# Performance work log

Measured on AMD Instinct MI355X. Metric: run time of the kernel, lower is better.

Reference implementation:

```python
import jax, jax.numpy as jnp
import numpy as np

H, NH, L, S, B, V = 512, 8, 6, 2048, 2, 32000
DH = H // NH
EPS = 1e-5


def posenc(h, s):
    pos = jnp.arange(s, dtype=jnp.float32)[:, None]
    div = jnp.power(10000.0, jnp.arange(0, h, 2, dtype=jnp.float32) / h)
    pe = jnp.zeros((s, h), dtype=jnp.float32)
    pe = pe.at[:, 0::2].set(jnp.sin(pos / div))
    pe = pe.at[:, 1::2].set(jnp.cos(pos / div))
    return pe


def layernorm(x, g, b):
    mu = jnp.mean(x, axis=-1, keepdims=True)
    var = jnp.mean(jnp.square(x - mu), axis=-1, keepdims=True)
    return (x - mu) * jax.lax.rsqrt(var + EPS) * g + b


def setup_inputs() -> dict:
    key = jax.random.key(0)
    ks = jax.random.split(key, 16)
    sc = 0.02
    return {
        "src": jax.random.randint(ks[0], (B, S), 0, V),
        "mask": jnp.ones((B, 1, 1, S), dtype=jnp.int32),
        "emb": jax.random.normal(ks[1], (V, H), jnp.float32) * sc,
        "Wq": jax.random.normal(ks[2], (L, H, H), jnp.float32) * sc,
        "bq": jnp.zeros((L, H), jnp.float32),
        "Wk": jax.random.normal(ks[3], (L, H, H), jnp.float32) * sc,
        "bk": jnp.zeros((L, H), jnp.float32),
        "Wv": jax.random.normal(ks[4], (L, H, H), jnp.float32) * sc,
        "bv": jnp.zeros((L, H), jnp.float32),
        "Wo": jax.random.normal(ks[5], (L, H, H), jnp.float32) * sc,
        "bo": jnp.zeros((L, H), jnp.float32),
        "gamma": jnp.ones((L, H), jnp.float32),
        "beta": jnp.zeros((L, H), jnp.float32),
        "W1": jax.random.normal(ks[6], (L, H, 4 * H), jnp.float32) * sc,
        "b1": jnp.zeros((L, 4 * H), jnp.float32),
        "W2": jax.random.normal(ks[7], (L, 4 * H, H), jnp.float32) * sc,
        "b2": jnp.zeros((L, H), jnp.float32),
    }


def reference(src, mask, emb, Wq, bq, Wk, bk, Wv, bv, Wo, bo, gamma, beta, W1, b1, W2, b2):
    x = emb[src] + posenc(H, S)[None, :, :]  # [B,S,H]
    for i in range(L):
        q = (x @ Wq[i] + bq[i]).reshape(B, S, NH, DH).transpose(0, 2, 1, 3)
        k = (x @ Wk[i] + bk[i]).reshape(B, S, NH, DH).transpose(0, 2, 1, 3)
        v = (x @ Wv[i] + bv[i]).reshape(B, S, NH, DH).transpose(0, 2, 1, 3)
        scores = jnp.einsum("bhqd,bhkd->bhqk", q, k) / jnp.sqrt(jnp.float32(DH))
        scores = jnp.where(mask == 0, jnp.float32(-1e20), scores)
        attn = jax.nn.softmax(scores, axis=-1)
        av = jnp.einsum("bhqk,bhkd->bhqd", attn, v)
        attn_out = av.transpose(0, 2, 1, 3).reshape(B, S, H) @ Wo[i] + bo[i]
        # NOTE: same LayerNorm params applied to both sublayers (as in source)
        res = x + layernorm(attn_out, gamma[i], beta[i])
        ffn = jax.nn.relu(res @ W1[i] + b1[i]) @ W2[i] + b2[i]
        x = res + layernorm(ffn, gamma[i], beta[i])
    return x
```

## Files before the change

kernel.cpp:

```cpp
#include <hip/hip_runtime.h>
#include <math.h>

#define HDIM 512
#define NHEAD 8
#define NLAYER 6
#define SEQ 2048
#define BATCH 2
#define DHEAD 64
#define TOKENS (BATCH*SEQ)
#define FFND (4*HDIM)
#define QSTR 1536

typedef unsigned short u16;
typedef unsigned long long u64;
typedef __attribute__((ext_vector_type(8))) short short8;
typedef __attribute__((ext_vector_type(4))) float f32x4;

__device__ __forceinline__ u16 f2b(float f) {
  unsigned u = __float_as_uint(f);
  u += 0x7FFFu + ((u >> 16) & 1u);
  return (u16)(u >> 16);
}

__device__ __forceinline__ unsigned cvtpk_bf16(float lo, float hi) {
  unsigned r;
  asm("v_cvt_pk_bf16_f32 %0, %1, %2" : "=v"(r) : "v"(lo), "v"(hi));
  return r;
}

__device__ __forceinline__ void gload_lds16(const u16* g, u16* l) {
  __builtin_amdgcn_global_load_lds((const __attribute__((address_space(1))) void*)g,
                                   (__attribute__((address_space(3))) void*)l, 16, 0, 0);
}

__global__ void embed_pe(const int* __restrict__ src, const float* __restrict__ emb,
                         float* __restrict__ X, u16* __restrict__ Xb) {
  int tok = blockIdx.x;
  int lane = threadIdx.x;
  int s = tok & (SEQ - 1);
  int c0 = lane * 8;
  const float* e = emb + (long)src[tok] * HDIM + c0;
  float v[8];
#pragma unroll
  for (int j = 0; j < 8; j++) {
    int c = c0 + j;
    float arg = (float)s * exp2f(-(float)(c & ~1) * 0.02595256917f);
    v[j] = e[j] + ((c & 1) ? cosf(arg) : sinf(arg));
  }
  float* xp = X + (long)tok * HDIM + c0;
#pragma unroll
  for (int j = 0; j < 8; j++) xp[j] = v[j];
  u16 hb[8];
#pragma unroll
  for (int j = 0; j < 8; j++) hb[j] = f2b(v[j]);
  uint4 pk;
  pk.x = hb[0] | ((unsigned)hb[1] << 16);
  pk.y = hb[2] | ((unsigned)hb[3] << 16);
  pk.z = hb[4] | ((unsigned)hb[5] << 16);
  pk.w = hb[6] | ((unsigned)hb[7] << 16);
  *(uint4*)(Xb + (long)tok * HDIM + c0) = pk;
}

__global__ void maskprep(const int* __restrict__ mask, u64* __restrict__ mb) {
  int t = threadIdx.x;
  int b = t >> 5, tile = t & 31;
  const int* m = mask + b * SEQ + tile * 64;
  u64 w = 0;
#pragma unroll
  for (int j = 0; j < 64; j++) w |= (u64)(m[j] != 0) << j;
  mb[t] = w;
}

__global__ __launch_bounds__(256) void prep_weights(
    const float* __restrict__ Wq, const float* __restrict__ Wk, const float* __restrict__ Wv,
    const float* __restrict__ Wo, const float* __restrict__ W1, const float* __restrict__ W2,
    const float* __restrict__ bq, const float* __restrict__ bk, const float* __restrict__ bv,
    u16* __restrict__ Wqkvt, u16* __restrict__ Wot, u16* __restrict__ W1t, u16* __restrict__ W2t,
    float* __restrict__ bqkv) {
  int t = blockIdx.x;
  int tid = threadIdx.x;
  if (t == 768) {
    for (int i = tid; i < 1536; i += 256)
      bqkv[i] = (i < 512) ? bq[i] : (i < 1024) ? bk[i - 512] : bv[i - 1024];
    return;
  }
  const float* src; u16* dst; int K, N, kt, nt; long drow0 = 0;
  if (t < 192)      { int m = t / 64, r = t % 64; src = (m==0)?Wq:(m==1)?Wk:Wv; dst = Wqkvt; drow0 = (long)m*512; K=512;  N=512;  kt=r/8;  nt=r%8; }
  else if (t < 256) { int r = t - 192; src = Wo; dst = Wot; K=512;  N=512;  kt=r/8;  nt=r%8; }
  else if (t < 512) { int r = t - 256; src = W1; dst = W1t; K=512;  N=2048; kt=r/32; nt=r%32; }
  else              { int r = t - 512; src = W2; dst = W2t; K=2048; N=512;  kt=r/8;  nt=r%8; }
  __shared__ __align__(16) u16 Lt[64 * 72];
  int kl = tid >> 2;
#pragma unroll
  for (int rr = 0; rr < 4; rr++) {
    int cl = (tid & 3) * 4 + rr * 16;
    float4 v = *(const float4*)(src + (long)(kt * 64 + kl) * N + nt * 64 + cl);
    Lt[(cl + 0) * 72 + kl] = f2b(v.x);
    Lt[(cl + 1) * 72 + kl] = f2b(v.y);
    Lt[(cl + 2) * 72 + kl] = f2b(v.z);
    Lt[(cl + 3) * 72 + kl] = f2b(v.w);
  }
  __syncthreads();
  int nl = tid >> 2;
  int kc = (tid & 3) * 16;
  u16* dp = dst + (drow0 + nt * 64 + nl) * (long)K + kt * 64 + kc;
  *(uint4*)dp       = *(const uint4*)&Lt[nl * 72 + kc];
  *(uint4*)(dp + 8) = *(const uint4*)&Lt[nl * 72 + kc + 8];
}

__global__ __launch_bounds__(256) void vtranspose(const u16* __restrict__ QKV,
                                                  u16* __restrict__ Vtb) {
  __shared__ __align__(16) u16 Lt[64 * 72];
  int tid = threadIdx.x;
  int bh = blockIdx.y, b = bh >> 3, h = bh & 7;
  int s0 = blockIdx.x * 64;
  const u16* vsrc = QKV + (long)(b * SEQ + s0) * QSTR + 1024 + h * DHEAD;
  int key = tid >> 2, dc = (tid & 3) * 16;
  const u16* vp = vsrc + (long)key * QSTR + dc;
  uint4 v0 = *(const uint4*)vp;
  uint4 v1 = *(const uint4*)(vp + 8);
  unsigned vr[8] = { v0.x, v0.y, v0.z, v0.w, v1.x, v1.y, v1.z, v1.w };
#pragma unroll
  for (int j = 0; j < 8; j++) {
    Lt[(dc + 2 * j) * 72 + key]     = (u16)vr[j];
    Lt[(dc + 2 * j + 1) * 72 + key] = (u16)(vr[j] >> 16);
  }
  __syncthreads();
  int d = tid >> 2, kc = (tid & 3) * 16;
  u16* dst = Vtb + ((long)bh * DHEAD + d) * SEQ + s0 + kc;
  *(uint4*)dst       = *(const uint4*)&Lt[d * 72 + kc];
  *(uint4*)(dst + 8) = *(const uint4*)&Lt[d * 72 + kc + 8];
}

template <int BN, int KSPLIT, bool RELU, bool WF32, bool WB16>
__global__ __launch_bounds__(256) void gemm_tn(const u16* __restrict__ A,
                                               const u16* __restrict__ Bt,
                                               const float* __restrict__ bias,
                                               float* __restrict__ Cf,
                                               u16* __restrict__ Cb,
                                               int M, int N, int K) {
  constexpr int NF = BN / 32;
  __shared__ __align__(16) u16 As[2][128 * 32];
  __shared__ __align__(16) u16 Bs[2][BN * 32];
  int tid = threadIdx.x;
  int wave = tid >> 6, lane = tid & 63;
  int ln = lane & 15, hi = lane >> 4;
  int wm = wave >> 1, wn = wave & 1;
  int m0 = blockIdx.y * 128, n0 = blockIdx.x * BN;
  int z = (KSPLIT > 1) ? blockIdx.z : 0;
  int Ks = K / KSPLIT;
  const u16* Ab = A + z * Ks;
  const u16* Bb = Bt + z * Ks;

  f32x4 acc[4][NF] = {};

  int srow = lane >> 2;
  int skc  = (lane & 3) * 8;

  auto issue = [&](int kt, int buf) {
    int k0 = kt * 32;
#pragma unroll
    for (int j = 0; j < 2; j++) {
      int row = (wave * 2 + j) * 16 + srow;
      gload_lds16(Ab + (long)(m0 + row) * K + k0 + skc, &As[buf][row * 32 + skc]);
    }
#pragma unroll
    for (int j = 0; j < BN / 64; j++) {
      int row = (wave * (BN / 64) + j) * 16 + srow;
      gload_lds16(Bb + (long)(n0 + row) * K + k0 + skc, &Bs[buf][row * 32 + skc]);
    }
  };

  int NT = Ks / 32;
  issue(0, 0);
  __syncthreads();
  for (int kt = 0; kt < NT; kt++) {
    int buf = kt & 1;
    if (kt + 1 < NT) issue(kt + 1, buf ^ 1);
    short8 af[4], bf[NF];
#pragma unroll
    for (int mt = 0; mt < 4; mt++)
      af[mt] = *(const short8*)&As[buf][(wm * 64 + mt * 16 + ln) * 32 + 8 * hi];
#pragma unroll
    for (int nt = 0; nt < NF; nt++)
      bf[nt] = *(const short8*)&Bs[buf][(wn * (BN / 2) + nt * 16 + ln) * 32 + 8 * hi];
#pragma unroll
    for (int mt = 0; mt < 4; mt++)
#pragma unroll
      for (int nt = 0; nt < NF; nt++)
        acc[mt][nt] = __builtin_amdgcn_mfma_f32_16x16x32_bf16(af[mt], bf[nt], acc[mt][nt], 0, 0, 0);
    __syncthreads();
  }

  float* Cz = WF32 ? (Cf + (long)z * M * N) : nullptr;
#pragma unroll
  for (int mt = 0; mt < 4; mt++)
#pragma unroll
    for (int nt = 0; nt < NF; nt++)
#pragma unroll
      for (int r = 0; r < 4; r++) {
        int row = m0 + wm * 64 + mt * 16 + hi * 4 + r;
        int col = n0 + wn * (BN / 2) + nt * 16 + ln;
        float v = acc[mt][nt][r];
        if (KSPLIT == 1 || z == 0) v += bias[col];
        if (RELU) v = fmaxf(v, 0.0f);
        if (WF32) Cz[(long)row * N + col] = v;
        if (WB16) Cb[(long)row * N + col] = f2b(v);
      }
}

__global__ __launch_bounds__(256) void attention(const u16* __restrict__ QKV,
                                                 const u16* __restrict__ Vtb,
                                                 const u64* __restrict__ maskb,
                                                 float* __restrict__ Opart,
                                                 float* __restrict__ Lpart) {
  __shared__ __align__(16) u16 Ks[2][64 * 64];
  __shared__ __align__(16) u16 Vs[2][64 * 64];
  __shared__ u64 Msk[SEQ / 64];
  int tid = threadIdx.x, w = tid >> 6, lane = tid & 63;
  int ln = lane & 15, hi = lane >> 4;
  int h0 = hi & 1, h1 = hi >> 1, ln7 = ln & 7;
  int lin = blockIdx.x;
  int lid = (lin & 7) * 128 + (lin >> 3);
  int bh = lid >> 6, qt = (lid >> 1) & 31, kz = lid & 1;
  int b = bh >> 3, h = bh & 7;
  int q0 = qt * 64 + w * 16;
  const u16* qbase = QKV + (long)b * SEQ * QSTR + h * DHEAD;
  const u16* kbase = qbase + 512;
  const u16* vtbase = Vtb + (long)bh * DHEAD * SEQ;

  short8 qf[2];
#pragma unroll
  for (int ks = 0; ks < 2; ks++)
    qf[ks] = *(const short8*)(qbase + (long)(q0 + ln) * QSTR + ks * 32 + 8 * hi);

  u64 mw0 = 0;
  if (tid < SEQ / 64) mw0 = maskb[b * (SEQ / 64) + tid];

  int sr0 = tid >> 3, sc = tid & 7;
  const u16 *kp0, *kp1, *vp0, *vp1;
  {
    int r1 = sr0 + 32;
    int key0 = (sr0 & 7) | ((sr0 & 0x18) << 1) | ((sr0 & 0x20) >> 2);
    int key1 = (r1 & 7) | ((r1 & 0x18) << 1) | ((r1 & 0x20) >> 2);
    kp0 = kbase + (long)key0 * QSTR + (sc ^ (sr0 & 7)) * 8;
    kp1 = kbase + (long)key1 * QSTR + (sc ^ (r1 & 7)) * 8;
    vp0 = vtbase + (long)sr0 * SEQ + (sc ^ (sr0 & 7)) * 8;
    vp1 = vtbase + (long)r1 * SEQ + (sc ^ (r1 & 7)) * 8;
  }
  int d0 = sr0 * 64 + sc * 8, d1 = d0 + 2048;

  auto issue = [&](int t, int buf) {
    long ko = (long)t * (64 * QSTR);
    int vo = t * 64;
    gload_lds16(kp0 + ko, &Ks[buf][d0]);
    gload_lds16(kp1 + ko, &Ks[buf][d1]);
    gload_lds16(vp0 + vo, &Vs[buf][d0]);
    gload_lds16(vp1 + vo, &Vs[buf][d1]);
  };

  f32x4 o[4] = {};
  float lsum = 0.0f;
  const int t0 = kz * 16;
  const int NTL = 16;

  issue(t0, 0);
  issue(t0 + 1, 1);
  if (tid < SEQ / 64) Msk[tid] = mw0;
  asm volatile("s_waitcnt vmcnt(4)" ::: "memory");
  __builtin_amdgcn_sched_barrier(0);
  __builtin_amdgcn_s_barrier();
  __builtin_amdgcn_sched_barrier(0);

  for (int ti = 0; ti < NTL; ti++) {
    int buf = ti & 1;
    u64 mw = Msk[t0 + ti];

    f32x4 s[4] = {};
#pragma unroll
    for (int ks = 0; ks < 2; ks++)
#pragma unroll
      for (int kb = 0; kb < 4; kb++) {
        short8 kf = *(const short8*)&Ks[buf][(kb * 16 + ln) * 64 + (((ks << 2) + hi) ^ ln7) * 8];
        s[kb] = __builtin_amdgcn_mfma_f32_16x16x32_bf16(kf, qf[ks], s[kb], 0, 0, 0);
      }

    unsigned D[4][2];
    if (mw == 0xFFFFFFFFFFFFFFFFull) {
#pragma unroll
      for (int kb = 0; kb < 4; kb++) {
        float p[4];
#pragma unroll
        for (int r = 0; r < 4; r++) {
          float pv = __expf(s[kb][r] * 0.125f);
          lsum += pv;
          p[r] = pv;
        }
        D[kb][0] = cvtpk_bf16(p[0], p[1]);
        D[kb][1] = cvtpk_bf16(p[2], p[3]);
      }
    } else {
      unsigned shb = h1 * 16 + h0 * 4;
      u64 mws = mw >> shb;
      unsigned nib[4] = { (unsigned)mws & 0xFu, (unsigned)(mws >> 32) & 0xFu,
                          (unsigned)(mws >> 8) & 0xFu, (unsigned)(mws >> 40) & 0xFu };
#pragma unroll
      for (int kb = 0; kb < 4; kb++) {
        float p[4];
#pragma unroll
        for (int r = 0; r < 4; r++) {
          float pv = __expf(s[kb][r] * 0.125f);
          pv = ((nib[kb] >> r) & 1u) ? pv : 0.0f;
          lsum += pv;
          p[r] = pv;
        }
        D[kb][0] = cvtpk_bf16(p[0], p[1]);
        D[kb][1] = cvtpk_bf16(p[2], p[3]);
      }
    }

    short8 pb[2];
#pragma unroll
    for (int ks = 0; ks < 2; ks++) {
      unsigned own0 = h0 ? D[2 + ks][0] : D[ks][0];
      unsigned own1 = h0 ? D[2 + ks][1] : D[ks][1];
      unsigned snd0 = h0 ? D[ks][0] : D[2 + ks][0];
      unsigned snd1 = h0 ? D[ks][1] : D[2 + ks][1];
      unsigned rc0 = (unsigned)__shfl_xor((int)snd0, 16);
      unsigned rc1 = (unsigned)__shfl_xor((int)snd1, 16);
      union { unsigned u[4]; short8 v; } pu;
      pu.u[0] = h0 ? rc0 : own0;
      pu.u[1] = h0 ? rc1 : own1;
      pu.u[2] = h0 ? own0 : rc0;
      pu.u[3] = h0 ? own1 : rc1;
      pb[ks] = pu.v;
    }

#pragma unroll
    for (int ks = 0; ks < 2; ks++)
#pragma unroll
      for (int mb = 0; mb < 4; mb++) {
        short8 vf = *(const short8*)&Vs[buf][(mb * 16 + ln) * 64 + (((ks << 2) + hi) ^ ln7) * 8];
        o[mb] = __builtin_amdgcn_mfma_f32_16x16x32_bf16(vf, pb[ks], o[mb], 0, 0, 0);
      }

    asm volatile("s_waitcnt lgkmcnt(0)" ::: "memory");
    __builtin_amdgcn_sched_barrier(0);
    __builtin_amdgcn_s_barrier();
    __builtin_amdgcn_sched_barrier(0);
    if (ti + 2 < NTL) {
      issue(t0 + ti + 2, buf);
      asm volatile("s_waitcnt vmcnt(4)" ::: "memory");
    } else {
      asm volatile("s_waitcnt vmcnt(0)" ::: "memory");
    }
    __builtin_amdgcn_sched_barrier(0);
    __builtin_amdgcn_s_barrier();
    __builtin_amdgcn_sched_barrier(0);
  }

  lsum += __shfl_xor(lsum, 16);
  lsum += __shfl_xor(lsum, 32);

  float* OpB = Opart + (long)lid * 4096 + w * 1024;
#pragma unroll
  for (int mb = 0; mb < 4; mb++)
    *(f32x4*)&OpB[ln * 64 + mb * 16 + hi * 4] = o[mb];
  if (hi == 0) Lpart[(long)lid * 64 + w * 16 + ln] = lsum;
}

__global__ __launch_bounds__(256) void attn_merge(const float* __restrict__ Op,
                                                  const float* __restrict__ Lp,
                                                  u16* __restrict__ Og) {
  int lin = blockIdx.x;
  int mlid = (lin & 7) * 64 + (lin >> 3);
  int bh = mlid >> 5, qt = mlid & 31;
  int b = bh >> 3, h = bh & 7;
  int tid = threadIdx.x;
  __shared__ float Ls[64];
  if (tid < 64) Ls[tid] = 1.0f / (Lp[(long)mlid * 128 + tid] + Lp[(long)mlid * 128 + 64 + tid]);
  __syncthreads();
  const float* P0 = Op + (long)mlid * 8192;
  const float* P1 = P0 + 4096;
  u16* obase = Og + (long)b * SEQ * HDIM + (long)qt * 64 * HDIM + h * DHEAD;
#pragma unroll
  for (int j = 0; j < 4; j++) {
    int flat = j * 1024 + tid * 4;
    int row = flat >> 6, c = flat & 63;
    float4 a = *(const float4*)&P0[flat];
    float4 bb = *(const float4*)&P1[flat];
    float rl = Ls[row];
    uint2 val;
    val.x = cvtpk_bf16((a.x + bb.x) * rl, (a.y + bb.y) * rl);
    val.y = cvtpk_bf16((a.z + bb.z) * rl, (a.w + bb.w) * rl);
    *(uint2*)(obase + (long)row * HDIM + c) = val;
  }
}

__global__ __launch_bounds__(256) void ln_residual(const float* __restrict__ Xin,
                                                   const float* __restrict__ T0,
                                                   const float* __restrict__ T1,
                                                   const float* __restrict__ gamma,
                                                   const float* __restrict__ beta,
                                                   float* __restrict__ Xout,
                                                   u16* __restrict__ Xb) {
  int tid = threadIdx.x, w = tid >> 6, lane = tid & 63;
  int row = blockIdx.x * 4 + w;
  const float* t0 = T0 + (long)row * HDIM;
  const float* t1 = T1 + (long)row * HDIM;
  int c0 = lane * 8;
  float v[8];
  {
    float4 a0 = *(const float4*)(t0 + c0);
    float4 b0 = *(const float4*)(t0 + c0 + 4);
    float4 a1 = *(const float4*)(t1 + c0);
    float4 b1 = *(const float4*)(t1 + c0 + 4);
    v[0] = a0.x + a1.x; v[1] = a0.y + a1.y; v[2] = a0.z + a1.z; v[3] = a0.w + a1.w;
    v[4] = b0.x + b1.x; v[5] = b0.y + b1.y; v[6] = b0.z + b1.z; v[7] = b0.w + b1.w;
  }
  float sum = 0.0f;
#pragma unroll
  for (int j = 0; j < 8; j++) sum += v[j];
#pragma unroll
  for (int off = 32; off; off >>= 1) sum += __shfl_xor(sum, off);
  float mu = sum * (1.0f / HDIM);
  float sq = 0.0f;
#pragma unroll
  for (int j = 0; j < 8; j++) { float d = v[j] - mu; sq += d * d; }
#pragma unroll
  for (int off = 32; off; off >>= 1) sq += __shfl_xor(sq, off);
  float rs = rsqrtf(sq * (1.0f / HDIM) + 1e-5f);
  const float* xin = Xin + (long)row * HDIM + c0;
  float* xout = Xout + (long)row * HDIM + c0;
  u16 hb[8];
#pragma unroll
  for (int j = 0; j < 8; j++) {
    int c = c0 + j;
    float y = xin[j] + (v[j] - mu) * rs * gamma[c] + beta[c];
    xout[j] = y;
    hb[j] = f2b(y);
  }
  uint4 pk;
  pk.x = hb[0] | ((unsigned)hb[1] << 16);
  pk.y = hb[2] | ((unsigned)hb[3] << 16);
  pk.z = hb[4] | ((unsigned)hb[5] << 16);
  pk.w = hb[6] | ((unsigned)hb[7] << 16);
  *(uint4*)(Xb + (long)row * HDIM + c0) = pk;
}

extern "C" void kernel_launch(void* const* d_in, const int* in_sizes, int n_in,
                              void* d_out, int out_size, void* d_ws, size_t ws_size,
                              hipStream_t stream) {
  const int*   src   = (const int*)d_in[0];
  const int*   mask  = (const int*)d_in[1];
  const float* emb   = (const float*)d_in[2];
  const float* Wq    = (const float*)d_in[3];
  const float* bq    = (const float*)d_in[4];
  const float* Wk    = (const float*)d_in[5];
  const float* bk    = (const float*)d_in[6];
  const float* Wv    = (const float*)d_in[7];
  const float* bv    = (const float*)d_in[8];
  const float* Wo    = (const float*)d_in[9];
  const float* bo    = (const float*)d_in[10];
  const float* gamma = (const float*)d_in[11];
  const float* beta  = (const float*)d_in[12];
  const float* W1    = (const float*)d_in[13];
  const float* b1    = (const float*)d_in[14];
  const float* W2    = (const float*)d_in[15];
  const float* b2    = (const float*)d_in[16];

  char* ws = (char*)d_ws;
  float* X     = (float*)(ws);
  u16*   Xb    = (u16*)(ws + (8ll << 20));
  u16*   QKVb  = (u16*)(ws + (12ll << 20));
  u16*   Mb    = (u16*)(ws + (12ll << 20));
  u16*   AVb   = (u16*)(ws + (24ll << 20));
  float* T     = (float*)(ws + (28ll << 20));
  u16*   Wqkvt = (u16*)(ws + (44ll << 20));
  u16*   Wot   = (u16*)(ws + (45ll << 20) + (512ll << 10));
  u16*   W1t   = (u16*)(ws + (46ll << 20));
  u16*   W2t   = (u16*)(ws + (48ll << 20));
  float* bqkv  = (float*)(ws + (50ll << 20));
  float* Lpart = (float*)(ws + (50ll << 20) + (512ll << 10));
  u16*   Vtb   = (u16*)(ws + (51ll << 20));
  u64*   maskbits = (u64*)(ws + (55ll << 20));
  float* Opart = T;
  float* T1    = T + (long)TOKENS * HDIM;

  embed_pe<<<dim3(TOKENS), dim3(64), 0, stream>>>(src, emb, X, Xb);
  maskprep<<<dim3(1), dim3(64), 0, stream>>>(mask, maskbits);

  for (int i = 0; i < NLAYER; i++) {
    long wo = (long)i * HDIM * HDIM;
    prep_weights<<<dim3(769), 256, 0, stream>>>(
        Wq + wo, Wk + wo, Wv + wo, Wo + wo,
        W1 + (long)i * HDIM * FFND, W2 + (long)i * FFND * HDIM,
        bq + i * HDIM, bk + i * HDIM, bv + i * HDIM,
        Wqkvt, Wot, W1t, W2t, bqkv);

    gemm_tn<128, 1, false, false, true><<<dim3(QSTR / 128, TOKENS / 128), 256, 0, stream>>>(
        Xb, Wqkvt, bqkv, nullptr, QKVb, TOKENS, QSTR, HDIM);

    vtranspose<<<dim3(SEQ / 64, BATCH * NHEAD), 256, 0, stream>>>(QKVb, Vtb);

    attention<<<dim3(1024), 256, 0, stream>>>(QKVb, Vtb, maskbits, Opart, Lpart);

    attn_merge<<<dim3(512), 256, 0, stream>>>(Opart, Lpart, AVb);

    gemm_tn<64, 2, false, true, false><<<dim3(HDIM / 64, TOKENS / 128, 2), 256, 0, stream>>>(
        AVb, Wot, bo + i * HDIM, T, nullptr, TOKENS, HDIM, HDIM);

    ln_residual<<<dim3(TOKENS / 4), 256, 0, stream>>>(X, T, T1, gamma + i * HDIM,
                                                      beta + i * HDIM, X, Xb);

    gemm_tn<128, 1, true, false, true><<<dim3(FFND / 128, TOKENS / 128), 256, 0, stream>>>(
        Xb, W1t, b1 + (long)i * FFND, nullptr, Mb, TOKENS, FFND, HDIM);

    gemm_tn<64, 2, false, true, false><<<dim3(HDIM / 64, TOKENS / 128, 2), 256, 0, stream>>>(
        Mb, W2t, b2 + i * HDIM, T, nullptr, TOKENS, HDIM, FFND);

    ln_residual<<<dim3(TOKENS / 4), 256, 0, stream>>>(X, T, T1, gamma + i * HDIM,
                                                      beta + i * HDIM, X, Xb);
  }

  hipMemcpyAsync(d_out, X, (size_t)TOKENS * HDIM * sizeof(float),
                 hipMemcpyDeviceToDevice, stream);
}
```

Measured before the change: 998.7 us.

## Fuse attention split merge via atomic counter and drop split-K in projection GEMMs

The separate attn_merge kernel is removed. The attention block that finishes second in each key-split pair now merges both partial outputs and writes the bf16 result. It uses a per-pair atomic counter, read by parity so the counter never has to be reset between layers. The Wo and W2 GEMMs drop split-K in favour of 64x64 tiles, so ln_residual reads one fp32 buffer instead of summing two partials. The attention MFMA sections are also wrapped in s_setprio. Together this cuts kernel launches and partial-sum traffic, at the cost of memory fences and atomics and less K-parallelism per GEMM block.

```diff
diff --git a/kernel.cpp b/kernel.cpp
--- a/kernel.cpp
+++ b/kernel.cpp
@@ -61,7 +61,8 @@
   *(uint4*)(Xb + (long)tok * HDIM + c0) = pk;
 }
 
-__global__ void maskprep(const int* __restrict__ mask, u64* __restrict__ mb) {
+__global__ void maskprep(const int* __restrict__ mask, u64* __restrict__ mb,
+                         int* __restrict__ cnt) {
   int t = threadIdx.x;
   int b = t >> 5, tile = t & 31;
   const int* m = mask + b * SEQ + tile * 64;
@@ -69,6 +70,8 @@
 #pragma unroll
   for (int j = 0; j < 64; j++) w |= (u64)(m[j] != 0) << j;
   mb[t] = w;
+#pragma unroll
+  for (int j = 0; j < 8; j++) cnt[t * 8 + j] = 0;
 }
 
 __global__ __launch_bounds__(256) void prep_weights(
@@ -132,7 +135,7 @@
   *(uint4*)(dst + 8) = *(const uint4*)&Lt[d * 72 + kc + 8];
 }
 
-template <int BN, int KSPLIT, bool RELU, bool WF32, bool WB16>
+template <int BM, int BN, int KSPLIT, bool RELU, bool WF32, bool WB16>
 __global__ __launch_bounds__(256) void gemm_tn(const u16* __restrict__ A,
                                                const u16* __restrict__ Bt,
                                                const float* __restrict__ bias,
@@ -140,19 +143,20 @@
                                                u16* __restrict__ Cb,
                                                int M, int N, int K) {
   constexpr int NF = BN / 32;
-  __shared__ __align__(16) u16 As[2][128 * 32];
+  constexpr int MF = BM / 32;
+  __shared__ __align__(16) u16 As[2][BM * 32];
   __shared__ __align__(16) u16 Bs[2][BN * 32];
   int tid = threadIdx.x;
   int wave = tid >> 6, lane = tid & 63;
   int ln = lane & 15, hi = lane >> 4;
   int wm = wave >> 1, wn = wave & 1;
-  int m0 = blockIdx.y * 128, n0 = blockIdx.x * BN;
+  int m0 = blockIdx.y * BM, n0 = blockIdx.x * BN;
   int z = (KSPLIT > 1) ? blockIdx.z : 0;
   int Ks = K / KSPLIT;
   const u16* Ab = A + z * Ks;
   const u16* Bb = Bt + z * Ks;
 
-  f32x4 acc[4][NF] = {};
+  f32x4 acc[MF][NF] = {};
 
   int srow = lane >> 2;
   int skc  = (lane & 3) * 8;
@@ -160,8 +164,8 @@
   auto issue = [&](int kt, int buf) {
     int k0 = kt * 32;
 #pragma unroll
-    for (int j = 0; j < 2; j++) {
-      int row = (wave * 2 + j) * 16 + srow;
+    for (int j = 0; j < BM / 64; j++) {
+      int row = (wave * (BM / 64) + j) * 16 + srow;
       gload_lds16(Ab + (long)(m0 + row) * K + k0 + skc, &As[buf][row * 32 + skc]);
     }
 #pragma unroll
@@ -177,15 +181,15 @@
   for (int kt = 0; kt < NT; kt++) {
     int buf = kt & 1;
     if (kt + 1 < NT) issue(kt + 1, buf ^ 1);
-    short8 af[4], bf[NF];
-#pragma unroll
-    for (int mt = 0; mt < 4; mt++)
-      af[mt] = *(const short8*)&As[buf][(wm * 64 + mt * 16 + ln) * 32 + 8 * hi];
+    short8 af[MF], bf[NF];
+#pragma unroll
+    for (int mt = 0; mt < MF; mt++)
+      af[mt] = *(const short8*)&As[buf][(wm * (BM / 2) + mt * 16 + ln) * 32 + 8 * hi];
 #pragma unroll
     for (int nt = 0; nt < NF; nt++)
       bf[nt] = *(const short8*)&Bs[buf][(wn * (BN / 2) + nt * 16 + ln) * 32 + 8 * hi];
 #pragma unroll
-    for (int mt = 0; mt < 4; mt++)
+    for (int mt = 0; mt < MF; mt++)
 #pragma unroll
       for (int nt = 0; nt < NF; nt++)
         acc[mt][nt] = __builtin_amdgcn_mfma_f32_16x16x32_bf16(af[mt], bf[nt], acc[mt][nt], 0, 0, 0);
@@ -194,12 +198,12 @@
 
   float* Cz = WF32 ? (Cf + (long)z * M * N) : nullptr;
 #pragma unroll
-  for (int mt = 0; mt < 4; mt++)
+  for (int mt = 0; mt < MF; mt++)
 #pragma unroll
     for (int nt = 0; nt < NF; nt++)
 #pragma unroll
       for (int r = 0; r < 4; r++) {
-        int row = m0 + wm * 64 + mt * 16 + hi * 4 + r;
+        int row = m0 + wm * (BM / 2) + mt * 16 + hi * 4 + r;
         int col = n0 + wn * (BN / 2) + nt * 16 + ln;
         float v = acc[mt][nt][r];
         if (KSPLIT == 1 || z == 0) v += bias[col];
@@ -213,10 +217,13 @@
                                                  const u16* __restrict__ Vtb,
                                                  const u64* __restrict__ maskb,
                                                  float* __restrict__ Opart,
-                                                 float* __restrict__ Lpart) {
+                                                 float* __restrict__ Lpart,
+                                                 int* __restrict__ cnt,
+                                                 u16* __restrict__ Og) {
   __shared__ __align__(16) u16 Ks[2][64 * 64];
   __shared__ __align__(16) u16 Vs[2][64 * 64];
   __shared__ u64 Msk[SEQ / 64];
+  __shared__ int oldv;
   int tid = threadIdx.x, w = tid >> 6, lane = tid & 63;
   int ln = lane & 15, hi = lane >> 4;
   int h0 = hi & 1, h1 = hi >> 1, ln7 = ln & 7;
@@ -277,6 +284,7 @@
     u64 mw = Msk[t0 + ti];
 
     f32x4 s[4] = {};
+    __builtin_amdgcn_s_setprio(1);
 #pragma unroll
     for (int ks = 0; ks < 2; ks++)
 #pragma unroll
@@ -284,6 +292,7 @@
         short8 kf = *(const short8*)&Ks[buf][(kb * 16 + ln) * 64 + (((ks << 2) + hi) ^ ln7) * 8];
         s[kb] = __builtin_amdgcn_mfma_f32_16x16x32_bf16(kf, qf[ks], s[kb], 0, 0, 0);
       }
+    __builtin_amdgcn_s_setprio(0);
 
     unsigned D[4][2];
     if (mw == 0xFFFFFFFFFFFFFFFFull) {
@@ -336,6 +345,7 @@
       pb[ks] = pu.v;
     }
 
+    __builtin_amdgcn_s_setprio(1);
 #pragma unroll
     for (int ks = 0; ks < 2; ks++)
 #pragma unroll
@@ -343,6 +353,7 @@
         short8 vf = *(const short8*)&Vs[buf][(mb * 16 + ln) * 64 + (((ks << 2) + hi) ^ ln7) * 8];
         o[mb] = __builtin_amdgcn_mfma_f32_16x16x32_bf16(vf, pb[ks], o[mb], 0, 0, 0);
       }
+    __builtin_amdgcn_s_setprio(0);
 
     asm volatile("s_waitcnt lgkmcnt(0)" ::: "memory");
     __builtin_amdgcn_sched_barrier(0);
@@ -367,39 +378,43 @@
   for (int mb = 0; mb < 4; mb++)
     *(f32x4*)&OpB[ln * 64 + mb * 16 + hi * 4] = o[mb];
   if (hi == 0) Lpart[(long)lid * 64 + w * 16 + ln] = lsum;
-}
-
-__global__ __launch_bounds__(256) void attn_merge(const float* __restrict__ Op,
-                                                  const float* __restrict__ Lp,
-                                                  u16* __restrict__ Og) {
-  int lin = blockIdx.x;
-  int mlid = (lin & 7) * 64 + (lin >> 3);
-  int bh = mlid >> 5, qt = mlid & 31;
-  int b = bh >> 3, h = bh & 7;
-  int tid = threadIdx.x;
-  __shared__ float Ls[64];
-  if (tid < 64) Ls[tid] = 1.0f / (Lp[(long)mlid * 128 + tid] + Lp[(long)mlid * 128 + 64 + tid]);
+
+  __threadfence();
   __syncthreads();
-  const float* P0 = Op + (long)mlid * 8192;
-  const float* P1 = P0 + 4096;
+  if (tid == 0) oldv = atomicAdd(&cnt[lid >> 1], 1);
+  __syncthreads();
+  if ((oldv & 1) == 0) return;
+  __threadfence();
+
+  int lidp = lid ^ 1;
+  const float* PpB = Opart + (long)lidp * 4096 + w * 1024;
+  float lp = Lpart[(long)lidp * 64 + w * 16 + ln];
+  float rl = 1.0f / (lsum + lp);
+
+  u16* Ot = &Ks[0][0] + w * 1024;
+#pragma unroll
+  for (int mb = 0; mb < 4; mb++) {
+    f32x4 po = *(const f32x4*)&PpB[ln * 64 + mb * 16 + hi * 4];
+    *(unsigned*)&Ot[ln * 64 + mb * 16 + hi * 4 + 0] =
+        cvtpk_bf16((o[mb][0] + po[0]) * rl, (o[mb][1] + po[1]) * rl);
+    *(unsigned*)&Ot[ln * 64 + mb * 16 + hi * 4 + 2] =
+        cvtpk_bf16((o[mb][2] + po[2]) * rl, (o[mb][3] + po[3]) * rl);
+  }
+  asm volatile("s_waitcnt lgkmcnt(0)" ::: "memory");
+  __builtin_amdgcn_s_barrier();
   u16* obase = Og + (long)b * SEQ * HDIM + (long)qt * 64 * HDIM + h * DHEAD;
 #pragma unroll
-  for (int j = 0; j < 4; j++) {
-    int flat = j * 1024 + tid * 4;
-    int row = flat >> 6, c = flat & 63;
-    float4 a = *(const float4*)&P0[flat];
-    float4 bb = *(const float4*)&P1[flat];
-    float rl = Ls[row];
-    uint2 val;
-    val.x = cvtpk_bf16((a.x + bb.x) * rl, (a.y + bb.y) * rl);
-    val.y = cvtpk_bf16((a.z + bb.z) * rl, (a.w + bb.w) * rl);
-    *(uint2*)(obase + (long)row * HDIM + c) = val;
+  for (int pass = 0; pass < 2; pass++) {
+    int row = (lane >> 3) + 8 * pass;
+    int c = lane & 7;
+    uint4 val = *(const uint4*)&Ot[(w * 16 + row) * 64 + c * 8 - w * 1024 + w * 1024];
+    val = *(const uint4*)&Ot[row * 64 + c * 8];
+    *(uint4*)(obase + (long)(w * 16 + row) * HDIM + c * 8) = val;
   }
 }
 
 __global__ __launch_bounds__(256) void ln_residual(const float* __restrict__ Xin,
                                                    const float* __restrict__ T0,
-                                                   const float* __restrict__ T1,
                                                    const float* __restrict__ gamma,
                                                    const float* __restrict__ beta,
                                                    float* __restrict__ Xout,
@@ -407,16 +422,13 @@
   int tid = threadIdx.x, w = tid >> 6, lane = tid & 63;
   int row = blockIdx.x * 4 + w;
   const float* t0 = T0 + (long)row * HDIM;
-  const float* t1 = T1 + (long)row * HDIM;
   int c0 = lane * 8;
   float v[8];
   {
     float4 a0 = *(const float4*)(t0 + c0);
     float4 b0 = *(const float4*)(t0 + c0 + 4);
-    float4 a1 = *(const float4*)(t1 + c0);
-    float4 b1 = *(const float4*)(t1 + c0 + 4);
-    v[0] = a0.x + a1.x; v[1] = a0.y + a1.y; v[2] = a0.z + a1.z; v[3] = a0.w + a1.w;
-    v[4] = b0.x + b1.x; v[5] = b0.y + b1.y; v[6] = b0.z + b1.z; v[7] = b0.w + b1.w;
+    v[0] = a0.x; v[1] = a0.y; v[2] = a0.z; v[3] = a0.w;
+    v[4] = b0.x; v[5] = b0.y; v[6] = b0.z; v[7] = b0.w;
   }
   float sum = 0.0f;
 #pragma unroll
@@ -484,11 +496,11 @@
   float* Lpart = (float*)(ws + (50ll << 20) + (512ll << 10));
   u16*   Vtb   = (u16*)(ws + (51ll << 20));
   u64*   maskbits = (u64*)(ws + (55ll << 20));
+  int*   cnt   = (int*)(ws + (55ll << 20) + 4096);
   float* Opart = T;
-  float* T1    = T + (long)TOKENS * HDIM;
 
   embed_pe<<<dim3(TOKENS), dim3(64), 0, stream>>>(src, emb, X, Xb);
-  maskprep<<<dim3(1), dim3(64), 0, stream>>>(mask, maskbits);
+  maskprep<<<dim3(1), dim3(64), 0, stream>>>(mask, maskbits, cnt);
 
   for (int i = 0; i < NLAYER; i++) {
     long wo = (long)i * HDIM * HDIM;
@@ -498,28 +510,26 @@
         bq + i * HDIM, bk + i * HDIM, bv + i * HDIM,
         Wqkvt, Wot, W1t, W2t, bqkv);
 
-    gemm_tn<128, 1, false, false, true><<<dim3(QSTR / 128, TOKENS / 128), 256, 0, stream>>>(
+    gemm_tn<128, 128, 1, false, false, true><<<dim3(QSTR / 128, TOKENS / 128), 256, 0, stream>>>(
         Xb, Wqkvt, bqkv, nullptr, QKVb, TOKENS, QSTR, HDIM);
 
     vtranspose<<<dim3(SEQ / 64, BATCH * NHEAD), 256, 0, stream>>>(QKVb, Vtb);
 
-    attention<<<dim3(1024), 256, 0, stream>>>(QKVb, Vtb, maskbits, Opart, Lpart);
-
-    attn_merge<<<dim3(512), 256, 0, stream>>>(Opart, Lpart, AVb);
-
-    gemm_tn<64, 2, false, true, false><<<dim3(HDIM / 64, TOKENS / 128, 2), 256, 0, stream>>>(
+    attention<<<dim3(1024), 256, 0, stream>>>(QKVb, Vtb, maskbits, Opart, Lpart, cnt, AVb);
+
+    gemm_tn<64, 64, 1, false, true, false><<<dim3(HDIM / 64, TOKENS / 64), 256, 0, stream>>>(
         AVb, Wot, bo + i * HDIM, T, nullptr, TOKENS, HDIM, HDIM);
 
-    ln_residual<<<dim3(TOKENS / 4), 256, 0, stream>>>(X, T, T1, gamma + i * HDIM,
+    ln_residual<<<dim3(TOKENS / 4), 256, 0, stream>>>(X, T, gamma + i * HDIM,
                                                       beta + i * HDIM, X, Xb);
 
-    gemm_tn<128, 1, true, false, true><<<dim3(FFND / 128, TOKENS / 128), 256, 0, stream>>>(
+    gemm_tn<128, 128, 1, true, false, true><<<dim3(FFND / 128, TOKENS / 128), 256, 0, stream>>>(
         Xb, W1t, b1 + (long)i * FFND, nullptr, Mb, TOKENS, FFND, HDIM);
 
-    gemm_tn<64, 2, false, true, false><<<dim3(HDIM / 64, TOKENS / 128, 2), 256, 0, stream>>>(
+    gemm_tn<64, 64, 1, false, true, false><<<dim3(HDIM / 64, TOKENS / 64), 256, 0, stream>>>(
         Mb, W2t, b2 + i * HDIM, T, nullptr, TOKENS, HDIM, FFND);
 
-    ln_residual<<<dim3(TOKENS / 4), 256, 0, stream>>>(X, T, T1, gamma + i * HDIM,
+    ln_residual<<<dim3(TOKENS / 4), 256, 0, stream>>>(X, T, gamma + i * HDIM,
                                                       beta + i * HDIM, X, Xb);
   }
 
```

After: 1.879 ms. +88.1%, slower.

## Replace split-K N=512 GEMMs with 64x64 tiles and add MFMA priority hints

Applied to the files above, without the earlier changes.

The Wo and W2 projections now use 64x64 output tiles with a full K loop (256 blocks) in place of a 2-way split-K over 128x64 tiles. This removes the second fp32 partial buffer and its extra read in ln_residual, which now reads one partial sum. The attention inner loop also raises wave priority around the MFMA blocks with s_setprio. The tradeoffs are lower per-block data reuse and the long K=2048 loop in the W2 GEMM running without split-K parallelism.

```diff
diff --git a/kernel.cpp b/kernel.cpp
--- a/kernel.cpp
+++ b/kernel.cpp
@@ -132,7 +132,7 @@
   *(uint4*)(dst + 8) = *(const uint4*)&Lt[d * 72 + kc + 8];
 }
 
-template <int BN, int KSPLIT, bool RELU, bool WF32, bool WB16>
+template <int BM, int BN, bool RELU, bool WF32, bool WB16>
 __global__ __launch_bounds__(256) void gemm_tn(const u16* __restrict__ A,
                                                const u16* __restrict__ Bt,
                                                const float* __restrict__ bias,
@@ -140,19 +140,16 @@
                                                u16* __restrict__ Cb,
                                                int M, int N, int K) {
   constexpr int NF = BN / 32;
-  __shared__ __align__(16) u16 As[2][128 * 32];
+  constexpr int MF = BM / 32;
+  __shared__ __align__(16) u16 As[2][BM * 32];
   __shared__ __align__(16) u16 Bs[2][BN * 32];
   int tid = threadIdx.x;
   int wave = tid >> 6, lane = tid & 63;
   int ln = lane & 15, hi = lane >> 4;
   int wm = wave >> 1, wn = wave & 1;
-  int m0 = blockIdx.y * 128, n0 = blockIdx.x * BN;
-  int z = (KSPLIT > 1) ? blockIdx.z : 0;
-  int Ks = K / KSPLIT;
-  const u16* Ab = A + z * Ks;
-  const u16* Bb = Bt + z * Ks;
-
-  f32x4 acc[4][NF] = {};
+  int m0 = blockIdx.y * BM, n0 = blockIdx.x * BN;
+
+  f32x4 acc[MF][NF] = {};
 
   int srow = lane >> 2;
   int skc  = (lane & 3) * 8;
@@ -160,51 +157,49 @@
   auto issue = [&](int kt, int buf) {
     int k0 = kt * 32;
 #pragma unroll
-    for (int j = 0; j < 2; j++) {
-      int row = (wave * 2 + j) * 16 + srow;
-      gload_lds16(Ab + (long)(m0 + row) * K + k0 + skc, &As[buf][row * 32 + skc]);
+    for (int j = 0; j < BM / 64; j++) {
+      int row = (wave * (BM / 64) + j) * 16 + srow;
+      gload_lds16(A + (long)(m0 + row) * K + k0 + skc, &As[buf][row * 32 + skc]);
     }
 #pragma unroll
     for (int j = 0; j < BN / 64; j++) {
       int row = (wave * (BN / 64) + j) * 16 + srow;
-      gload_lds16(Bb + (long)(n0 + row) * K + k0 + skc, &Bs[buf][row * 32 + skc]);
+      gload_lds16(Bt + (long)(n0 + row) * K + k0 + skc, &Bs[buf][row * 32 + skc]);
     }
   };
 
-  int NT = Ks / 32;
+  int NT = K / 32;
   issue(0, 0);
   __syncthreads();
   for (int kt = 0; kt < NT; kt++) {
     int buf = kt & 1;
     if (kt + 1 < NT) issue(kt + 1, buf ^ 1);
-    short8 af[4], bf[NF];
-#pragma unroll
-    for (int mt = 0; mt < 4; mt++)
-      af[mt] = *(const short8*)&As[buf][(wm * 64 + mt * 16 + ln) * 32 + 8 * hi];
+    short8 af[MF], bf[NF];
+#pragma unroll
+    for (int mt = 0; mt < MF; mt++)
+      af[mt] = *(const short8*)&As[buf][(wm * (BM / 2) + mt * 16 + ln) * 32 + 8 * hi];
 #pragma unroll
     for (int nt = 0; nt < NF; nt++)
       bf[nt] = *(const short8*)&Bs[buf][(wn * (BN / 2) + nt * 16 + ln) * 32 + 8 * hi];
 #pragma unroll
-    for (int mt = 0; mt < 4; mt++)
+    for (int mt = 0; mt < MF; mt++)
 #pragma unroll
       for (int nt = 0; nt < NF; nt++)
         acc[mt][nt] = __builtin_amdgcn_mfma_f32_16x16x32_bf16(af[mt], bf[nt], acc[mt][nt], 0, 0, 0);
     __syncthreads();
   }
 
-  float* Cz = WF32 ? (Cf + (long)z * M * N) : nullptr;
-#pragma unroll
-  for (int mt = 0; mt < 4; mt++)
+#pragma unroll
+  for (int mt = 0; mt < MF; mt++)
 #pragma unroll
     for (int nt = 0; nt < NF; nt++)
 #pragma unroll
       for (int r = 0; r < 4; r++) {
-        int row = m0 + wm * 64 + mt * 16 + hi * 4 + r;
+        int row = m0 + wm * (BM / 2) + mt * 16 + hi * 4 + r;
         int col = n0 + wn * (BN / 2) + nt * 16 + ln;
-        float v = acc[mt][nt][r];
-        if (KSPLIT == 1 || z == 0) v += bias[col];
+        float v = acc[mt][nt][r] + bias[col];
         if (RELU) v = fmaxf(v, 0.0f);
-        if (WF32) Cz[(long)row * N + col] = v;
+        if (WF32) Cf[(long)row * N + col] = v;
         if (WB16) Cb[(long)row * N + col] = f2b(v);
       }
 }
@@ -277,6 +272,7 @@
     u64 mw = Msk[t0 + ti];
 
     f32x4 s[4] = {};
+    __builtin_amdgcn_s_setprio(1);
 #pragma unroll
     for (int ks = 0; ks < 2; ks++)
 #pragma unroll
@@ -284,6 +280,7 @@
         short8 kf = *(const short8*)&Ks[buf][(kb * 16 + ln) * 64 + (((ks << 2) + hi) ^ ln7) * 8];
         s[kb] = __builtin_amdgcn_mfma_f32_16x16x32_bf16(kf, qf[ks], s[kb], 0, 0, 0);
       }
+    __builtin_amdgcn_s_setprio(0);
 
     unsigned D[4][2];
     if (mw == 0xFFFFFFFFFFFFFFFFull) {
@@ -336,6 +333,7 @@
       pb[ks] = pu.v;
     }
 
+    __builtin_amdgcn_s_setprio(1);
 #pragma unroll
     for (int ks = 0; ks < 2; ks++)
 #pragma unroll
@@ -343,6 +341,7 @@
         short8 vf = *(const short8*)&Vs[buf][(mb * 16 + ln) * 64 + (((ks << 2) + hi) ^ ln7) * 8];
         o[mb] = __builtin_amdgcn_mfma_f32_16x16x32_bf16(vf, pb[ks], o[mb], 0, 0, 0);
       }
+    __builtin_amdgcn_s_setprio(0);
 
     asm volatile("s_waitcnt lgkmcnt(0)" ::: "memory");
     __builtin_amdgcn_sched_barrier(0);
@@ -399,7 +398,6 @@
 
 __global__ __launch_bounds__(256) void ln_residual(const float* __restrict__ Xin,
                                                    const float* __restrict__ T0,
-                                                   const float* __restrict__ T1,
                                                    const float* __restrict__ gamma,
                                                    const float* __restrict__ beta,
                                                    float* __restrict__ Xout,
@@ -407,16 +405,13 @@
   int tid = threadIdx.x, w = tid >> 6, lane = tid & 63;
   int row = blockIdx.x * 4 + w;
   const float* t0 = T0 + (long)row * HDIM;
-  const float* t1 = T1 + (long)row * HDIM;
   int c0 = lane * 8;
   float v[8];
   {
     float4 a0 = *(const float4*)(t0 + c0);
     float4 b0 = *(const float4*)(t0 + c0 + 4);
-    float4 a1 = *(const float4*)(t1 + c0);
-    float4 b1 = *(const float4*)(t1 + c0 + 4);
-    v[0] = a0.x + a1.x; v[1] = a0.y + a1.y; v[2] = a0.z + a1.z; v[3] = a0.w + a1.w;
-    v[4] = b0.x + b1.x; v[5] = b0.y + b1.y; v[6] = b0.z + b1.z; v[7] = b0.w + b1.w;
+    v[0] = a0.x; v[1] = a0.y; v[2] = a0.z; v[3] = a0.w;
+    v[4] = b0.x; v[5] = b0.y; v[6] = b0.z; v[7] = b0.w;
   }
   float sum = 0.0f;
 #pragma unroll
@@ -485,7 +480,6 @@
   u16*   Vtb   = (u16*)(ws + (51ll << 20));
   u64*   maskbits = (u64*)(ws + (55ll << 20));
   float* Opart = T;
-  float* T1    = T + (long)TOKENS * HDIM;
 
   embed_pe<<<dim3(TOKENS), dim3(64), 0, stream>>>(src, emb, X, Xb);
   maskprep<<<dim3(1), dim3(64), 0, stream>>>(mask, maskbits);
@@ -498,7 +492,7 @@
         bq + i * HDIM, bk + i * HDIM, bv + i * HDIM,
         Wqkvt, Wot, W1t, W2t, bqkv);
 
-    gemm_tn<128, 1, false, false, true><<<dim3(QSTR / 128, TOKENS / 128), 256, 0, stream>>>(
+    gemm_tn<128, 128, false, false, true><<<dim3(QSTR / 128, TOKENS / 128), 256, 0, stream>>>(
         Xb, Wqkvt, bqkv, nullptr, QKVb, TOKENS, QSTR, HDIM);
 
     vtranspose<<<dim3(SEQ / 64, BATCH * NHEAD), 256, 0, stream>>>(QKVb, Vtb);
@@ -507,19 +501,19 @@
 
     attn_merge<<<dim3(512), 256, 0, stream>>>(Opart, Lpart, AVb);
 
-    gemm_tn<64, 2, false, true, false><<<dim3(HDIM / 64, TOKENS / 128, 2), 256, 0, stream>>>(
+    gemm_tn<64, 64, false, true, false><<<dim3(HDIM / 64, TOKENS / 64), 256, 0, stream>>>(
         AVb, Wot, bo + i * HDIM, T, nullptr, TOKENS, HDIM, HDIM);
 
-    ln_residual<<<dim3(TOKENS / 4), 256, 0, stream>>>(X, T, T1, gamma + i * HDIM,
+    ln_residual<<<dim3(TOKENS / 4), 256, 0, stream>>>(X, T, gamma + i * HDIM,
                                                       beta + i * HDIM, X, Xb);
 
-    gemm_tn<128, 1, true, false, true><<<dim3(FFND / 128, TOKENS / 128), 256, 0, stream>>>(
+    gemm_tn<128, 128, true, false, true><<<dim3(FFND / 128, TOKENS / 128), 256, 0, stream>>>(
         Xb, W1t, b1 + (long)i * FFND, nullptr, Mb, TOKENS, FFND, HDIM);
 
-    gemm_tn<64, 2, false, true, false><<<dim3(HDIM / 64, TOKENS / 128, 2), 256, 0, stream>>>(
+    gemm_tn<64, 64, false, true, false><<<dim3(HDIM / 64, TOKENS / 64), 256, 0, stream>>>(
         Mb, W2t, b2 + i * HDIM, T, nullptr, TOKENS, HDIM, FFND);
 
-    ln_residual<<<dim3(TOKENS / 4), 256, 0, stream>>>(X, T, T1, gamma + i * HDIM,
+    ln_residual<<<dim3(TOKENS / 4), 256, 0, stream>>>(X, T, gamma + i * HDIM,
                                                       beta + i * HDIM, X, Xb);
   }
 
```

Result: faster. 946.1 us (-5.3%).
